# Kernel optimization log

Hardware: AMD Instinct MI355X
Metric: run time of the kernel (lower is better)

Reference implementation:

```python
import math
import jax, jax.numpy as jnp
import numpy as np

ORIG, NEW, LPW = 16000, 22050, 6  # orig_freq, new_freq, lowpass_filter_width


def _filters():
    """Kaldi LinearResample filter bank: first input index + weights per output phase.

    Mirrors Resample._indices_and_weights exactly (computed statically in numpy
    since the frequencies are module constants).
    """
    base = math.gcd(ORIG, NEW)
    P = NEW // base           # output_samples (number of polyphase filters)
    stride = ORIG // base     # conv_stride (input samples per polyphase block)
    cutoff = 0.99 * 0.5 * min(ORIG, NEW)
    ww = LPW / (2.0 * cutoff)  # half window width in seconds
    out_t = np.arange(P, dtype=np.float64) / NEW
    min_i = np.ceil((out_t - ww) * ORIG)   # first_indices, per phase
    max_i = np.floor((out_t + ww) * ORIG)
    W = int((max_i - min_i + 1).max())     # max filter length (~13 taps)
    j = np.arange(W, dtype=np.float64)
    inp_i = min_i[:, None] + j[None, :]
    dt = inp_i / ORIG - out_t[:, None]
    w = np.zeros_like(dt)
    inside = np.abs(dt) < ww
    w[inside] = 0.5 * (1.0 + np.cos(2.0 * np.pi * cutoff / LPW * dt[inside]))
    zero = dt == 0.0
    nz = ~zero
    w[nz] *= np.sin(2.0 * np.pi * cutoff * dt[nz]) / (np.pi * dt[nz])
    w[zero] *= 2.0 * cutoff
    w /= ORIG
    return min_i.astype(np.int64), w.astype(np.float32), P, stride


def _num_out(n):
    """Resample._output_samples (Kaldi GetNumOutputSamples)."""
    tick = ORIG * NEW // math.gcd(ORIG, NEW)
    tpi, tpo = tick // ORIG, tick // NEW
    interval = n * tpi
    if interval <= 0:
        return 0
    last = interval // tpo
    if last * tpo == interval:
        last -= 1
    return last + 1


def setup_inputs() -> dict:
    key = jax.random.key(0)
    # [batch, time] = 8 examples of 60 s @ 16 kHz
    return {"waveforms": jax.random.normal(key, (8, 960000), dtype=jnp.float32)}


def reference(waveforms):
    # Fused gather/dot formulation of the polyphase conv1d/conv_transpose1d loop:
    # out[b, t] = sum_j weights[t % P, j] * x[first_idx[t % P] + (t // P) * stride + j]
    # with zero padding outside [0, n) — bit-identical math to the torch loop.
    fi, w, P, stride = _filters()
    B, n = waveforms.shape
    tot = _num_out(n)
    Wn = w.shape[1]
    t = np.arange(tot)
    phase = t % P
    base = fi[phase] + (t // P) * stride           # [tot]
    full = base[:, None] + np.arange(Wn)[None, :]  # [tot, Wn] input sample indices
    pad_l = max(0, -int(full.min()))
    pad_r = max(0, int(full.max()) - (n - 1))
    xp = jnp.pad(waveforms, ((0, 0), (pad_l, pad_r)))
    idx = jnp.asarray(full + pad_l)                # static gather indices
    gathered = xp[:, idx]                          # [B, tot, Wn]
    wt = jnp.asarray(w)[phase]                     # [tot, Wn]
    return jnp.einsum('btw,tw->bt', gathered, wt)
```

## Files before the change

### kernel.cpp

```cpp
#include <hip/hip_runtime.h>
#include <math.h>

#define ORIG_F 16000
#define NEW_F  22050
#define P      441
#define STRIDE 320
#define GPW    3
#define NG     147
#define W20    20
#define MBLK   24
#define MCH    125
#define BATCH  8
#define TILE_F 7700

#ifndef M_PI
#define M_PI 3.14159265358979323846
#endif

__device__ __forceinline__ int kaldi_fi_int(int p) {
    int q = (p * 320) / 441;
    int r = p * 320 - q * 441;
    return q - 6 + (r <= 26 ? 0 : 1);
}

__global__ void build_table20_f32(float* __restrict__ w20, int* __restrict__ gab) {
    int idx = blockIdx.x * blockDim.x + threadIdx.x;
    if (idx >= P * W20) return;
    int p = idx / W20;
    int j = idx - p * W20;
    int fi0 = kaldi_fi_int((p / GPW) * GPW);
    int ab = fi0 & ~3;
    if (j == 0 && (p % GPW) == 0) gab[p / GPW] = ab;
    int ii = ab + j;
    int num = ii * 22050 - p * 16000;
    float wf = 0.f;
    if (num == 0) {
        wf = 0.99f;
    } else if (num <= 133636 && num >= -133636) {
        float dt = (float)num * (1.0f / 352800000.0f);
        float hann = 0.5f * (1.0f + __cosf(2.0f * (float)M_PI * 1320.0f * dt));
        float s = __sinf(2.0f * (float)M_PI * 7920.0f * dt);
        wf = hann * s / ((float)M_PI * dt) * (1.0f / 16000.0f);
    }
    w20[idx] = wf;
}

__device__ __forceinline__ float dot20f(const float4& x0, const float4& x1,
                                        const float4& x2, const float4& x3,
                                        const float4& x4, const float4* w) {
    float p0 = x0.x * w[0].x;
    p0 = fmaf(x0.y, w[0].y, p0); p0 = fmaf(x0.z, w[0].z, p0); p0 = fmaf(x0.w, w[0].w, p0);
    float p1 = x1.x * w[1].x;
    p1 = fmaf(x1.y, w[1].y, p1); p1 = fmaf(x1.z, w[1].z, p1); p1 = fmaf(x1.w, w[1].w, p1);
    float p2 = x2.x * w[2].x;
    p2 = fmaf(x2.y, w[2].y, p2); p2 = fmaf(x2.z, w[2].z, p2); p2 = fmaf(x2.w, w[2].w, p2);
    float p3 = x3.x * w[3].x;
    p3 = fmaf(x3.y, w[3].y, p3); p3 = fmaf(x3.z, w[3].z, p3); p3 = fmaf(x3.w, w[3].w, p3);
    float p4 = x4.x * w[4].x;
    p4 = fmaf(x4.y, w[4].y, p4); p4 = fmaf(x4.z, w[4].z, p4); p4 = fmaf(x4.w, w[4].w, p4);
    return ((p0 + p1) + (p2 + p3)) + p4;
}

__global__ __launch_bounds__(448) void resample9_kernel(
    const float* __restrict__ x, const float* __restrict__ w20,
    const int* __restrict__ gab, float* __restrict__ out,
    int n, int tot)
{
    __shared__ float xt[TILE_F];

    const int b  = blockIdx.y;
    const int mc = blockIdx.x;
    const float* __restrict__ xb = x + (size_t)b * n;

    const int S4 = mc * (MBLK * STRIDE) - 8;

    for (int i4 = threadIdx.x; i4 < TILE_F / 4; i4 += 448) {
        const int gi = S4 + i4 * 4;
        float4 v;
        if (gi >= 0 && gi + 3 < n) {
            v = *(const float4*)(xb + gi);
        } else {
            float s[4];
            #pragma unroll
            for (int q = 0; q < 4; ++q) {
                int ii = gi + q;
                s[q] = (ii >= 0 && ii < n) ? xb[ii] : 0.f;
            }
            v = make_float4(s[0], s[1], s[2], s[3]);
        }
        *(float4*)(xt + i4 * 4) = v;
    }

    const int t = threadIdx.x;
    float4 w[15];
    int Lbase = 0;
    int tout = 0;
    const bool active = (t < P);
    if (active) {
        const int g     = t % NG;
        const int third = t / NG;
        const float4* wp = (const float4*)(w20 + g * (GPW * W20));
        #pragma unroll
        for (int i = 0; i < 15; ++i) w[i] = wp[i];
        Lbase = gab[g] + 8 + third * (8 * STRIDE);
        tout  = (mc * MBLK + third * 8) * P + GPW * g;
    }
    __syncthreads();

    if (active) {
        float* __restrict__ ob = out + (size_t)b * tot;
        #pragma unroll 1
        for (int k = 0; k < 8; ++k) {
            const float4* q4 = (const float4*)(xt + Lbase);
            float4 x0 = q4[0], x1 = q4[1], x2 = q4[2], x3 = q4[3], x4 = q4[4];
            float a0 = dot20f(x0, x1, x2, x3, x4, &w[0]);
            float a1 = dot20f(x0, x1, x2, x3, x4, &w[5]);
            float a2 = dot20f(x0, x1, x2, x3, x4, &w[10]);
            ob[tout]     = a0;
            ob[tout + 1] = a1;
            ob[tout + 2] = a2;
            Lbase += STRIDE; tout += P;
        }
    }
}

extern "C" void kernel_launch(void* const* d_in, const int* in_sizes, int n_in,
                              void* d_out, int out_size, void* d_ws, size_t ws_size,
                              hipStream_t stream) {
    const float* x = (const float*)d_in[0];
    float* out = (float*)d_out;

    const int n = in_sizes[0] / BATCH;

    long long interval = (long long)n * P;
    long long last = interval / STRIDE;
    if (last * STRIDE == interval) last -= 1;
    const int tot = (int)(last + 1);

    float* w20 = (float*)d_ws;
    int*   gab = (int*)((char*)d_ws + (size_t)P * W20 * sizeof(float));

    build_table20_f32<<<(P * W20 + 255) / 256, 256, 0, stream>>>(w20, gab);

    dim3 grid(MCH, BATCH);
    resample9_kernel<<<grid, 448, 0, stream>>>(x, w20, gab, out, n, tot);
}
```

Baseline: 37.23 us.

## Fuse filter-table build into resample kernel and read input directly from global

Drops the separate weight-table kernel launch. Each block now computes the 441x20 filter bank into shared memory, with the math simplified to a reciprocal instead of a divide. The input shared-memory tile is removed, so threads read the waveform with float4 loads straight from global memory and rely on cache reuse. Only the first and last chunks take a bounds-checked path. This saves one launch and the staging pass, but every block recomputes the trig weights, and the global loads are unaligned and overlapping.

```diff
diff --git a/kernel.cpp b/kernel.cpp
--- a/kernel.cpp
+++ b/kernel.cpp
@@ -1,8 +1,6 @@
 #include <hip/hip_runtime.h>
 #include <math.h>
 
-#define ORIG_F 16000
-#define NEW_F  22050
 #define P      441
 #define STRIDE 320
 #define GPW    3
@@ -11,7 +9,7 @@
 #define MBLK   24
 #define MCH    125
 #define BATCH  8
-#define TILE_F 7700
+#define NW     (P * W20)
 
 #ifndef M_PI
 #define M_PI 3.14159265358979323846
@@ -23,26 +21,18 @@
     return q - 6 + (r <= 26 ? 0 : 1);
 }
 
-__global__ void build_table20_f32(float* __restrict__ w20, int* __restrict__ gab) {
-    int idx = blockIdx.x * blockDim.x + threadIdx.x;
-    if (idx >= P * W20) return;
-    int p = idx / W20;
-    int j = idx - p * W20;
-    int fi0 = kaldi_fi_int((p / GPW) * GPW);
-    int ab = fi0 & ~3;
-    if (j == 0 && (p % GPW) == 0) gab[p / GPW] = ab;
-    int ii = ab + j;
-    int num = ii * 22050 - p * 16000;
+__device__ __forceinline__ float kaldi_w(int p, int ab, int j) {
+    int num = (ab + j) * 22050 - p * 16000;
     float wf = 0.f;
     if (num == 0) {
         wf = 0.99f;
     } else if (num <= 133636 && num >= -133636) {
-        float dt = (float)num * (1.0f / 352800000.0f);
-        float hann = 0.5f * (1.0f + __cosf(2.0f * (float)M_PI * 1320.0f * dt));
-        float s = __sinf(2.0f * (float)M_PI * 7920.0f * dt);
-        wf = hann * s / ((float)M_PI * dt) * (1.0f / 16000.0f);
+        float nf = (float)num;
+        float hann = 0.5f + 0.5f * __cosf(nf * (float)(2.0 * M_PI * 1320.0 / 352800000.0));
+        float s = __sinf(nf * (float)(2.0 * M_PI * 7920.0 / 352800000.0));
+        wf = hann * s * (float)(22050.0 / M_PI) * __builtin_amdgcn_rcpf(nf);
     }
-    w20[idx] = wf;
+    return wf;
 }
 
 __device__ __forceinline__ float dot20f(const float4& x0, const float4& x1,
@@ -61,57 +51,45 @@
     return ((p0 + p1) + (p2 + p3)) + p4;
 }
 
-__global__ __launch_bounds__(448) void resample9_kernel(
-    const float* __restrict__ x, const float* __restrict__ w20,
-    const int* __restrict__ gab, float* __restrict__ out,
-    int n, int tot)
+__global__ __launch_bounds__(448) void resample10_kernel(
+    const float* __restrict__ x, float* __restrict__ out, int n, int tot)
 {
-    __shared__ float xt[TILE_F];
+    __shared__ float sw[NW];
 
     const int b  = blockIdx.y;
     const int mc = blockIdx.x;
-    const float* __restrict__ xb = x + (size_t)b * n;
 
-    const int S4 = mc * (MBLK * STRIDE) - 8;
-
-    for (int i4 = threadIdx.x; i4 < TILE_F / 4; i4 += 448) {
-        const int gi = S4 + i4 * 4;
-        float4 v;
-        if (gi >= 0 && gi + 3 < n) {
-            v = *(const float4*)(xb + gi);
-        } else {
-            float s[4];
-            #pragma unroll
-            for (int q = 0; q < 4; ++q) {
-                int ii = gi + q;
-                s[q] = (ii >= 0 && ii < n) ? xb[ii] : 0.f;
-            }
-            v = make_float4(s[0], s[1], s[2], s[3]);
-        }
-        *(float4*)(xt + i4 * 4) = v;
-    }
-
-    const int t = threadIdx.x;
-    float4 w[15];
-    int Lbase = 0;
-    int tout = 0;
-    const bool active = (t < P);
-    if (active) {
-        const int g     = t % NG;
-        const int third = t / NG;
-        const float4* wp = (const float4*)(w20 + g * (GPW * W20));
-        #pragma unroll
-        for (int i = 0; i < 15; ++i) w[i] = wp[i];
-        Lbase = gab[g] + 8 + third * (8 * STRIDE);
-        tout  = (mc * MBLK + third * 8) * P + GPW * g;
+    for (int i = threadIdx.x; i < NW; i += 448) {
+        int p = i / W20;
+        int j = i - p * W20;
+        int g3 = p - (p % GPW);
+        int ab = kaldi_fi_int(g3) & ~3;
+        sw[i] = kaldi_w(p, ab, j);
     }
     __syncthreads();
 
-    if (active) {
-        float* __restrict__ ob = out + (size_t)b * tot;
-        #pragma unroll 1
+    const int t = threadIdx.x;
+    if (t >= P) return;
+    const int g     = t % NG;
+    const int third = t / NG;
+    const int ab = kaldi_fi_int(GPW * g) & ~3;
+
+    float4 w[15];
+    const float4* wp = (const float4*)(sw + g * (GPW * W20));
+    #pragma unroll
+    for (int i = 0; i < 15; ++i) w[i] = wp[i];
+
+    const float* __restrict__ xb = x + (size_t)b * n;
+    float* __restrict__ ob = out + (size_t)b * tot;
+
+    const int m0 = mc * MBLK + third * 8;
+    int base = ab + m0 * STRIDE;
+    int tout = m0 * P + GPW * g;
+
+    if (mc != 0 && mc != MCH - 1) {
+        #pragma unroll 2
         for (int k = 0; k < 8; ++k) {
-            const float4* q4 = (const float4*)(xt + Lbase);
+            const float4* q4 = (const float4*)(xb + base);
             float4 x0 = q4[0], x1 = q4[1], x2 = q4[2], x3 = q4[3], x4 = q4[4];
             float a0 = dot20f(x0, x1, x2, x3, x4, &w[0]);
             float a1 = dot20f(x0, x1, x2, x3, x4, &w[5]);
@@ -119,7 +97,35 @@
             ob[tout]     = a0;
             ob[tout + 1] = a1;
             ob[tout + 2] = a2;
-            Lbase += STRIDE; tout += P;
+            base += STRIDE; tout += P;
+        }
+    } else {
+        const unsigned slim = (unsigned)(n - W20);
+        for (int k = 0; k < 8; ++k) {
+            float4 x0, x1, x2, x3, x4;
+            if ((unsigned)base <= slim) {
+                const float4* q4 = (const float4*)(xb + base);
+                x0 = q4[0]; x1 = q4[1]; x2 = q4[2]; x3 = q4[3]; x4 = q4[4];
+            } else {
+                float xs[W20];
+                #pragma unroll
+                for (int j = 0; j < W20; ++j) {
+                    int ii = base + j;
+                    xs[j] = (ii >= 0 && ii < n) ? xb[ii] : 0.f;
+                }
+                x0 = make_float4(xs[0], xs[1], xs[2], xs[3]);
+                x1 = make_float4(xs[4], xs[5], xs[6], xs[7]);
+                x2 = make_float4(xs[8], xs[9], xs[10], xs[11]);
+                x3 = make_float4(xs[12], xs[13], xs[14], xs[15]);
+                x4 = make_float4(xs[16], xs[17], xs[18], xs[19]);
+            }
+            float a0 = dot20f(x0, x1, x2, x3, x4, &w[0]);
+            float a1 = dot20f(x0, x1, x2, x3, x4, &w[5]);
+            float a2 = dot20f(x0, x1, x2, x3, x4, &w[10]);
+            ob[tout]     = a0;
+            ob[tout + 1] = a1;
+            ob[tout + 2] = a2;
+            base += STRIDE; tout += P;
         }
     }
 }
@@ -137,11 +143,6 @@
     if (last * STRIDE == interval) last -= 1;
     const int tot = (int)(last + 1);
 
-    float* w20 = (float*)d_ws;
-    int*   gab = (int*)((char*)d_ws + (size_t)P * W20 * sizeof(float));
-
-    build_table20_f32<<<(P * W20 + 255) / 256, 256, 0, stream>>>(w20, gab);
-
     dim3 grid(MCH, BATCH);
-    resample9_kernel<<<grid, 448, 0, stream>>>(x, w20, gab, out, n, tot);
+    resample10_kernel<<<grid, 448, 0, stream>>>(x, out, n, tot);
 }
```

Result: slower. 43.00 us (+15.5%).

## Drop shared-memory tiling; read input directly from global with flat thread grid

Applied to the files above, without the earlier changes.

Replaces the block-level shared-memory tile of the input with direct per-thread float4 loads from global memory, relying on L1/L2 for reuse across neighbouring phase groups. Work is remapped to a flat 1D grid of 256-thread blocks with 6 output blocks per thread, which removes the __syncthreads and the idle threads of the 448-wide blocks. Output stores become nontemporal. This trades the explicit LDS staging for more global or cache traffic, and reads may be unaligned float4 loads when the base index is not a multiple of 4.

```diff
diff --git a/kernel.cpp b/kernel.cpp
--- a/kernel.cpp
+++ b/kernel.cpp
@@ -1,17 +1,14 @@
 #include <hip/hip_runtime.h>
 #include <math.h>
 
-#define ORIG_F 16000
-#define NEW_F  22050
 #define P      441
 #define STRIDE 320
 #define GPW    3
 #define NG     147
 #define W20    20
-#define MBLK   24
-#define MCH    125
+#define MPT    6
+#define MCH    500
 #define BATCH  8
-#define TILE_F 7700
 
 #ifndef M_PI
 #define M_PI 3.14159265358979323846
@@ -28,17 +25,15 @@
     if (idx >= P * W20) return;
     int p = idx / W20;
     int j = idx - p * W20;
-    int fi0 = kaldi_fi_int((p / GPW) * GPW);
-    int ab = fi0 & ~3;
+    int ab = kaldi_fi_int(p - (p % GPW)) & ~3;
     if (j == 0 && (p % GPW) == 0) gab[p / GPW] = ab;
-    int ii = ab + j;
-    int num = ii * 22050 - p * 16000;
+    int num = (ab + j) * 22050 - p * 16000;
     float wf = 0.f;
     if (num == 0) {
         wf = 0.99f;
     } else if (num <= 133636 && num >= -133636) {
         float dt = (float)num * (1.0f / 352800000.0f);
-        float hann = 0.5f * (1.0f + __cosf(2.0f * (float)M_PI * 1320.0f * dt));
+        float hann = 0.5f + 0.5f * __cosf(2.0f * (float)M_PI * 1320.0f * dt);
         float s = __sinf(2.0f * (float)M_PI * 7920.0f * dt);
         wf = hann * s / ((float)M_PI * dt) * (1.0f / 16000.0f);
     }
@@ -61,66 +56,56 @@
     return ((p0 + p1) + (p2 + p3)) + p4;
 }
 
-__global__ __launch_bounds__(448) void resample9_kernel(
+__global__ __launch_bounds__(256) void resample11_kernel(
     const float* __restrict__ x, const float* __restrict__ w20,
     const int* __restrict__ gab, float* __restrict__ out,
     int n, int tot)
 {
-    __shared__ float xt[TILE_F];
+    int tid = blockIdx.x * blockDim.x + threadIdx.x;
+    if (tid >= BATCH * MCH * NG) return;
+    int g    = tid % NG;
+    int rest = tid / NG;
+    int mc   = rest % MCH;
+    int b    = rest / MCH;
 
-    const int b  = blockIdx.y;
-    const int mc = blockIdx.x;
     const float* __restrict__ xb = x + (size_t)b * n;
+    float* __restrict__ ob = out + (size_t)b * tot;
 
-    const int S4 = mc * (MBLK * STRIDE) - 8;
+    const float4* wp = (const float4*)(w20 + g * (GPW * W20));
+    float4 w[15];
+    #pragma unroll
+    for (int i = 0; i < 15; ++i) w[i] = wp[i];
 
-    for (int i4 = threadIdx.x; i4 < TILE_F / 4; i4 += 448) {
-        const int gi = S4 + i4 * 4;
-        float4 v;
-        if (gi >= 0 && gi + 3 < n) {
-            v = *(const float4*)(xb + gi);
+    const int ab = gab[g];
+    int base = ab + mc * MPT * STRIDE;
+    int t    = mc * MPT * P + g * GPW;
+
+    #pragma unroll 2
+    for (int k = 0; k < MPT; ++k) {
+        float4 x0, x1, x2, x3, x4;
+        if (base >= 0 && base + W20 <= n) {
+            const float4* q = (const float4*)(xb + base);
+            x0 = q[0]; x1 = q[1]; x2 = q[2]; x3 = q[3]; x4 = q[4];
         } else {
-            float s[4];
+            float xs[W20];
             #pragma unroll
-            for (int q = 0; q < 4; ++q) {
-                int ii = gi + q;
-                s[q] = (ii >= 0 && ii < n) ? xb[ii] : 0.f;
+            for (int j = 0; j < W20; ++j) {
+                int ii = base + j;
+                xs[j] = (ii >= 0 && ii < n) ? xb[ii] : 0.f;
             }
-            v = make_float4(s[0], s[1], s[2], s[3]);
+            x0 = make_float4(xs[0], xs[1], xs[2], xs[3]);
+            x1 = make_float4(xs[4], xs[5], xs[6], xs[7]);
+            x2 = make_float4(xs[8], xs[9], xs[10], xs[11]);
+            x3 = make_float4(xs[12], xs[13], xs[14], xs[15]);
+            x4 = make_float4(xs[16], xs[17], xs[18], xs[19]);
         }
-        *(float4*)(xt + i4 * 4) = v;
-    }
-
-    const int t = threadIdx.x;
-    float4 w[15];
-    int Lbase = 0;
-    int tout = 0;
-    const bool active = (t < P);
-    if (active) {
-        const int g     = t % NG;
-        const int third = t / NG;
-        const float4* wp = (const float4*)(w20 + g * (GPW * W20));
-        #pragma unroll
-        for (int i = 0; i < 15; ++i) w[i] = wp[i];
-        Lbase = gab[g] + 8 + third * (8 * STRIDE);
-        tout  = (mc * MBLK + third * 8) * P + GPW * g;
-    }
-    __syncthreads();
-
-    if (active) {
-        float* __restrict__ ob = out + (size_t)b * tot;
-        #pragma unroll 1
-        for (int k = 0; k < 8; ++k) {
-            const float4* q4 = (const float4*)(xt + Lbase);
-            float4 x0 = q4[0], x1 = q4[1], x2 = q4[2], x3 = q4[3], x4 = q4[4];
-            float a0 = dot20f(x0, x1, x2, x3, x4, &w[0]);
-            float a1 = dot20f(x0, x1, x2, x3, x4, &w[5]);
-            float a2 = dot20f(x0, x1, x2, x3, x4, &w[10]);
-            ob[tout]     = a0;
-            ob[tout + 1] = a1;
-            ob[tout + 2] = a2;
-            Lbase += STRIDE; tout += P;
-        }
+        float a0 = dot20f(x0, x1, x2, x3, x4, &w[0]);
+        float a1 = dot20f(x0, x1, x2, x3, x4, &w[5]);
+        float a2 = dot20f(x0, x1, x2, x3, x4, &w[10]);
+        __builtin_nontemporal_store(a0, &ob[t]);
+        __builtin_nontemporal_store(a1, &ob[t + 1]);
+        __builtin_nontemporal_store(a2, &ob[t + 2]);
+        base += STRIDE; t += P;
     }
 }
 
@@ -142,6 +127,7 @@
 
     build_table20_f32<<<(P * W20 + 255) / 256, 256, 0, stream>>>(w20, gab);
 
-    dim3 grid(MCH, BATCH);
-    resample9_kernel<<<grid, 448, 0, stream>>>(x, w20, gab, out, n, tot);
+    const int nthreads = BATCH * MCH * NG;
+    const int nblk = (nthreads + 255) / 256;
+    resample11_kernel<<<nblk, 256, 0, stream>>>(x, w20, gab, out, n, tot);
 }
```

Measured after the change: 32.58 us. 12.5% less time.
